# Optimization experiments

Hardware: AMD Instinct MI355X
Metric: run time of the kernel (lower is better)

The kernel has to match this reference:

```python
import jax, jax.numpy as jnp
import numpy as np

NG = 1024      # graphs
NPG = 128      # nodes per graph (forced by lin1 = Linear(128*hid, 128))
N = NG * NPG   # 131072 nodes
DEG = 16       # avg in-graph degree
E = N * DEG    # 2,097,152 edges
IN, H = 4, 64


def setup_inputs() -> dict:
    key = jax.random.key(0)
    ks = jax.random.split(key, 24)
    x = jax.random.normal(ks[0], (N, IN), jnp.float32)
    # edges constrained within each 128-node graph
    src = jax.random.randint(ks[1], (E,), 0, NPG)
    dst = jax.random.randint(ks[2], (E,), 0, NPG)
    off = jnp.repeat(jnp.arange(NG, dtype=jnp.int32) * NPG, NPG * DEG)
    edge_index = jnp.stack([src.astype(jnp.int32) + off, dst.astype(jnp.int32) + off])
    g = lambda k, shp, fan: jax.random.normal(k, shp, jnp.float32) / np.float32(np.sqrt(fan))
    return {
        "x": x, "edge_index": edge_index,
        # GATv2Conv(4->64)
        "Wl": g(ks[3], (IN, H), IN), "bl": jnp.zeros((H,), jnp.float32),
        "Wr": g(ks[4], (IN, H), IN), "br": jnp.zeros((H,), jnp.float32),
        "att_v2": g(ks[5], (H,), H), "b_v2": jnp.zeros((H,), jnp.float32),
        # GATConv #1 (64->64)
        "Wg1": g(ks[6], (H, H), H), "as1": g(ks[7], (H,), H),
        "ad1": g(ks[8], (H,), H), "bg1": jnp.zeros((H,), jnp.float32),
        # GATConv #2 (64->64)
        "Wg2": g(ks[9], (H, H), H), "as2": g(ks[10], (H,), H),
        "ad2": g(ks[11], (H,), H), "bg2": jnp.zeros((H,), jnp.float32),
        # LayerNorm(64)
        "ln_g": jnp.ones((H,), jnp.float32), "ln_b": jnp.zeros((H,), jnp.float32),
        # heads: Linear(128*64 -> 128), Linear(128 -> 1)
        "W1": g(ks[12], (NPG * H, 128), NPG * H), "b1": jnp.zeros((128,), jnp.float32),
        "W2": g(ks[13], (128, 1), 128), "b2": jnp.zeros((1,), jnp.float32),
    }


def _seg_softmax(logits, seg):
    # stable softmax over edges grouped by destination node
    m = jax.ops.segment_max(logits, seg, num_segments=N)
    ex = jnp.exp(logits - m[seg])
    s = jax.ops.segment_sum(ex, seg, num_segments=N)
    return ex / (s[seg] + 1e-16)


def _gatv2(x, src, dst, Wl, bl, Wr, br, att, bias):
    xl = x @ Wl + bl                       # source transform [N,H]
    xr = x @ Wr + br                       # target transform [N,H]
    e = jax.nn.leaky_relu(xl[src] + xr[dst], 0.2) @ att   # [E]
    a = _seg_softmax(e, dst)
    out = jax.ops.segment_sum(a[:, None] * xl[src], dst, num_segments=N)
    return out + bias


def _gat(x, src, dst, W, a_src, a_dst, bias):
    # GATConv default: add self-loops
    loop = jnp.arange(N, dtype=src.dtype)
    s2 = jnp.concatenate([src, loop]); d2 = jnp.concatenate([dst, loop])
    xw = x @ W                             # [N,H]
    al_s = xw @ a_src; al_d = xw @ a_dst   # per-node attention halves [N]
    e = jax.nn.leaky_relu(al_s[s2] + al_d[d2], 0.2)
    a = _seg_softmax(e, d2)
    out = jax.ops.segment_sum(a[:, None] * xw[s2], d2, num_segments=N)
    return out + bias


def _layernorm(x, g, b, eps=1e-5):
    mu = jnp.mean(x, -1, keepdims=True)
    var = jnp.mean(jnp.square(x - mu), -1, keepdims=True)
    return (x - mu) * jax.lax.rsqrt(var + eps) * g + b


def reference(x, edge_index, Wl, bl, Wr, br, att_v2, b_v2,
              Wg1, as1, ad1, bg1, Wg2, as2, ad2, bg2,
              ln_g, ln_b, W1, b1, W2, b2):
    src, dst = edge_index[0], edge_index[1]
    h = jax.nn.leaky_relu(_gatv2(x, src, dst, Wl, bl, Wr, br, att_v2, b_v2), 0.01)
    h = _layernorm(h, ln_g, ln_b)
    h = jax.nn.relu(_gat(h, src, dst, Wg1, as1, ad1, bg1))
    h = jax.nn.relu(_gat(h, src, dst, Wg2, as2, ad2, bg2))
    # linearize: batch is sorted with exactly NPG nodes per graph -> reshape
    h = h.reshape(NG, NPG * H)
    h = jax.nn.leaky_relu(h @ W1 + b1, 0.01)
    return jax.nn.sigmoid(h @ W2 + b2)     # [NG, 1]
```

## Files before the change

### kernel.cpp

```cpp
#include <hip/hip_runtime.h>
#include <hip/hip_bf16.h>

#define NGRAPH 1024
#define NPG 128
#define NTOT (NGRAPH*NPG)
#define EPG 2048
#define ETOT (NTOT*16)
#define HD 64

typedef unsigned int uint;
typedef unsigned short ushort_t;
typedef __attribute__((ext_vector_type(8))) short s8v;
typedef __attribute__((ext_vector_type(4))) float f32x4;

#define MFMA16 __builtin_amdgcn_mfma_f32_16x16x32_bf16

__device__ __forceinline__ float lrelu(float x, float s){ return fmaxf(x, x*s); }
__device__ __forceinline__ float b2lo(uint u){ return __uint_as_float(u << 16); }
__device__ __forceinline__ float b2hi(uint u){ return __uint_as_float(u & 0xFFFF0000u); }
__device__ __forceinline__ uint pkbf(float a, float b){
  union { __hip_bfloat162 h; uint u; } t;
  t.h = __hip_bfloat162{__float2bfloat16(a), __float2bfloat16(b)};
  return t.u;
}
__device__ __forceinline__ ushort_t bfb(float v){
  __hip_bfloat16 h = __float2bfloat16(v);
  union { __hip_bfloat16 h; ushort_t u; } t; t.h = h; return t.u;
}
union U4S8 { uint4 u; s8v s; };
__device__ __forceinline__ s8v bcs8(uint4 u){ U4S8 t; t.u = u; return t.s; }

#define DPP_ADD(v, ctrl) ((v) + __int_as_float(__builtin_amdgcn_update_dpp(0, __float_as_int(v), (ctrl), 0xF, 0xF, false)))

__device__ __forceinline__ int oswz(int r, int p){ return (r<<5) | ((((p>>2) ^ (r & 7))<<2) | (p & 3)); }
__device__ __forceinline__ int obase(int r, int oc){ return (r<<5) | (((oc) ^ (r & 7))<<2); }
__device__ __forceinline__ int sstg(int r, int c){ return (r<<5) | ((c ^ r) & 31); }

#define O_F   0
#define O_W   4096
#define O_EV  6144
#define O_ED  7168
#define O_X   8192
#define O_SOF 8704
#define O_SPO 8833
#define O_NMV 8961
#define O_SSE 9089
#define O_ALS 9217
#define O_ALD 9345
#define O_WAS 9476
#define O_WAD 9540
#define SM_SZ 9604

#define GF16(s, a) { \
    uint4 q0 = *(uint4*)&SM[O_F + obase((s), 2*qf+0)]; \
    uint4 q1 = *(uint4*)&SM[O_F + obase((s), 2*qf+1)]; \
    c0.x += (a)*b2lo(q0.x); c0.y += (a)*b2hi(q0.x); c0.z += (a)*b2lo(q0.y); c0.w += (a)*b2hi(q0.y); \
    c1.x += (a)*b2lo(q0.z); c1.y += (a)*b2hi(q0.z); c1.z += (a)*b2lo(q0.w); c1.w += (a)*b2hi(q0.w); \
    c2.x += (a)*b2lo(q1.x); c2.y += (a)*b2hi(q1.x); c2.z += (a)*b2lo(q1.y); c2.w += (a)*b2hi(q1.y); \
    c3.x += (a)*b2lo(q1.z); c3.y += (a)*b2hi(q1.z); c3.z += (a)*b2lo(q1.w); c3.w += (a)*b2hi(q1.w); }

#define STF16(d) { \
    sXl[oswz((d), qf*8+0)] = pkbf(c0.x,c0.y); sXl[oswz((d), qf*8+1)] = pkbf(c0.z,c0.w); \
    sXl[oswz((d), qf*8+2)] = pkbf(c1.x,c1.y); sXl[oswz((d), qf*8+3)] = pkbf(c1.z,c1.w); \
    sXl[oswz((d), qf*8+4)] = pkbf(c2.x,c2.y); sXl[oswz((d), qf*8+5)] = pkbf(c2.z,c2.w); \
    sXl[oswz((d), qf*8+6)] = pkbf(c3.x,c3.y); sXl[oswz((d), qf*8+7)] = pkbf(c3.z,c3.w); }
#define STG16(d) { \
    stg[sstg((d), qf*8+0)] = pkbf(c0.x,c0.y); stg[sstg((d), qf*8+1)] = pkbf(c0.z,c0.w); \
    stg[sstg((d), qf*8+2)] = pkbf(c1.x,c1.y); stg[sstg((d), qf*8+3)] = pkbf(c1.z,c1.w); \
    stg[sstg((d), qf*8+4)] = pkbf(c2.x,c2.y); stg[sstg((d), qf*8+5)] = pkbf(c2.z,c2.w); \
    stg[sstg((d), qf*8+6)] = pkbf(c3.x,c3.y); stg[sstg((d), qf*8+7)] = pkbf(c3.z,c3.w); }

__global__ void __launch_bounds__(256, 4) gnn_fused(
    const float* __restrict__ x, const int* __restrict__ ei,
    const float* __restrict__ Wl, const float* __restrict__ bl,
    const float* __restrict__ Wr, const float* __restrict__ br,
    const float* __restrict__ att, const float* __restrict__ bv2,
    const float* __restrict__ Wg1, const float* __restrict__ as1,
    const float* __restrict__ ad1, const float* __restrict__ bg1,
    const float* __restrict__ Wg2, const float* __restrict__ as2,
    const float* __restrict__ ad2, const float* __restrict__ bg2,
    const float* __restrict__ lng, const float* __restrict__ lnb,
    uint* __restrict__ hout)
{
  __shared__ uint SM[SM_SZ];
  uint*      sXl  = SM + O_F;
  _Float16*  evh  = (_Float16*)(SM + O_EV);
  ushort_t*  edsd = (ushort_t*)(SM + O_ED);
  int*       soff = (int*)(SM + O_SOF);
  int*       spos = (int*)(SM + O_SPO);
  float*     nmv  = (float*)(SM + O_NMV);
  float*     sse  = (float*)(SM + O_SSE);
  float*     als  = (float*)(SM + O_ALS);
  float*     ald  = (float*)(SM + O_ALD);
  float*     was  = (float*)(SM + O_WAS);
  float*     wad  = (float*)(SM + O_WAD);
  ushort_t*  sH16 = (ushort_t*)(SM + O_F);
  ushort_t*  wg16 = (ushort_t*)(SM + O_W);
  float*     lgf  = (float*)(SM + O_W);
  uint*      stg  = SM + O_W;

  const int g    = blockIdx.x;
  const int tid  = threadIdx.x;
  const int lane = tid & 63;
  const int wv   = tid >> 6;
  const int lw   = lane & 15;
  const int lq   = lane >> 4;
  const int oc   = lane & 7;
  const int ebase = g * EPG;

  if (tid < NPG) spos[tid] = 0;
  __syncthreads();
  for (int e = tid; e < EPG; e += 256)
    atomicAdd(&spos[ei[ETOT + ebase + e] - g*NPG], 1);
  __syncthreads();
  if (wv == 0) {
    int c0 = spos[lane], c1 = spos[lane + 64];
    #pragma unroll
    for (int o = 1; o < 64; o <<= 1) { int t = __shfl_up(c0, o); if (lane >= o) c0 += t; }
    #pragma unroll
    for (int o = 1; o < 64; o <<= 1) { int t = __shfl_up(c1, o); if (lane >= o) c1 += t; }
    int tot0 = __shfl(c0, 63);
    soff[lane + 1]  = c0;
    soff[lane + 65] = c1 + tot0;
    if (lane == 0) soff[0] = 0;
  }
  __syncthreads();
  if (tid < NPG) spos[tid] = soff[tid];
  __syncthreads();
  for (int e = tid; e < EPG; e += 256) {
    int s = ei[ebase + e] - g*NPG;
    int d = ei[ETOT + ebase + e] - g*NPG;
    int p = atomicAdd(&spos[d], 1);
    edsd[p] = (ushort_t)(s | (d << 8));
  }

  {
    const float4* x4g = (const float4*)x + (size_t)g * NPG;
    float4* sx4w = (float4*)(SM + O_X);
    if (tid < NPG) sx4w[tid] = x4g[tid];
    const int pl = lane & 31, hb = lane >> 5;
    const float2 wl0 = *(const float2*)&Wl[0*64 + 2*pl];
    const float2 wl1 = *(const float2*)&Wl[1*64 + 2*pl];
    const float2 wl2 = *(const float2*)&Wl[2*64 + 2*pl];
    const float2 wl3 = *(const float2*)&Wl[3*64 + 2*pl];
    const float2 blp = *(const float2*)&bl[2*pl];
    for (int st = 0; st < 16; st++) {
      int i = st*8 + wv*2 + hb;
      float4 xi = x4g[i];
      float l0 = blp.x + xi.x*wl0.x + xi.y*wl1.x + xi.z*wl2.x + xi.w*wl3.x;
      float l1 = blp.y + xi.x*wl0.y + xi.y*wl1.y + xi.z*wl2.y + xi.w*wl3.y;
      sXl[oswz(i, pl)] = pkbf(l0, l1);
    }
  }
  __syncthreads();

  {
    const float4* sx4 = (const float4*)(SM + O_X);
    const int g16 = tid >> 4;
    float4 w0 = *(const float4*)&Wr[0*64 + lw*4];
    float4 w1 = *(const float4*)&Wr[1*64 + lw*4];
    float4 w2 = *(const float4*)&Wr[2*64 + lw*4];
    float4 w3 = *(const float4*)&Wr[3*64 + lw*4];
    float4 brv = *(const float4*)&br[lw*4];
    float4 atv = *(const float4*)&att[lw*4];
    for (int it = 0; it < 8; it++) {
      int d = it*16 + g16;
      float4 xd = sx4[d];
      float4 xr;
      xr.x = brv.x + xd.x*w0.x + xd.y*w1.x + xd.z*w2.x + xd.w*w3.x;
      xr.y = brv.y + xd.x*w0.y + xd.y*w1.y + xd.z*w2.y + xd.w*w3.y;
      xr.z = brv.z + xd.x*w0.z + xd.y*w1.z + xd.z*w2.z + xd.w*w3.z;
      xr.w = brv.w + xd.x*w0.w + xd.y*w1.w + xd.z*w2.w + xd.w*w3.w;
      int p0 = soff[d], p1 = soff[d+1];
      for (int p = p0; p < p1; p++) {
        int s = edsd[p] & 127;
        uint2 ql = *(uint2*)&SM[O_F + oswz(s, 2*lw)];
        float e, v;
        v = b2lo(ql.x)+xr.x; e  = lrelu(v,0.2f)*atv.x;
        v = b2hi(ql.x)+xr.y; e += lrelu(v,0.2f)*atv.y;
        v = b2lo(ql.y)+xr.z; e += lrelu(v,0.2f)*atv.z;
        v = b2hi(ql.y)+xr.w; e += lrelu(v,0.2f)*atv.w;
        e = DPP_ADD(e, 0x111); e = DPP_ADD(e, 0x112);
        e = DPP_ADD(e, 0x114); e = DPP_ADD(e, 0x118);
        if (lw == 15) lgf[p] = e;
      }
    }
  }
  __syncthreads();

  {
    const int g16 = tid >> 4, sl = tid & 15;
    for (int it = 0; it < 8; it++) {
      int d = it*16 + g16;
      int p0 = soff[d], p1 = soff[d+1];
      float m = -1e30f;
      for (int p = p0 + sl; p < p1; p += 16) m = fmaxf(m, lgf[p]);
      #pragma unroll
      for (int o = 1; o < 16; o <<= 1) m = fmaxf(m, __shfl_xor(m, o));
      float ssum = 0.f;
      for (int p = p0 + sl; p < p1; p += 16) {
        float ex = __expf(lgf[p] - m); ssum += ex; evh[p] = (_Float16)ex;
      }
      #pragma unroll
      for (int o = 1; o < 16; o <<= 1) ssum += __shfl_xor(ssum, o);
      if (sl == 0) nmv[d] = 1.f / (ssum + 1e-16f);
    }
  }
  __syncthreads();

  {
    const int rr = tid >> 2, qf = tid & 3;
    auto doRow = [&](int d, int toStage) {
      int p0 = soff[d], p1 = soff[d+1];
      float nmv_d = nmv[d];
      f32x4 c0={0,0,0,0}, c1={0,0,0,0}, c2={0,0,0,0}, c3={0,0,0,0};
      for (int p = p0; p < p1; p++) {
        int s = edsd[p] & 127;
        float a = nmv_d * (float)evh[p];
        GF16(s, a)
      }
      float s1 = 0.f, s2 = 0.f;
      #define BRELN(cv, j) { \
        float4 bq = *(const float4*)&bv2[qf*16 + 4*(j)]; \
        cv.x = lrelu(cv.x + bq.x, 0.01f); cv.y = lrelu(cv.y + bq.y, 0.01f); \
        cv.z = lrelu(cv.z + bq.z, 0.01f); cv.w = lrelu(cv.w + bq.w, 0.01f); \
        s1 += cv.x + cv.y + cv.z + cv.w; \
        s2 += cv.x*cv.x + cv.y*cv.y + cv.z*cv.z + cv.w*cv.w; }
      BRELN(c0,0) BRELN(c1,1) BRELN(c2,2) BRELN(c3,3)
      #undef BRELN
      s1 += __shfl_xor(s1, 1); s2 += __shfl_xor(s2, 1);
      s1 += __shfl_xor(s1, 2); s2 += __shfl_xor(s2, 2);
      float mu  = s1 * 0.015625f;
      float var = s2 * 0.015625f - mu*mu;
      float rs  = rsqrtf(var + 1e-5f);
      #define LNAP(cv, j) { \
        float4 gq = *(const float4*)&lng[qf*16 + 4*(j)]; \
        float4 bq = *(const float4*)&lnb[qf*16 + 4*(j)]; \
        cv.x = (cv.x-mu)*rs*gq.x + bq.x; cv.y = (cv.y-mu)*rs*gq.y + bq.y; \
        cv.z = (cv.z-mu)*rs*gq.z + bq.z; cv.w = (cv.w-mu)*rs*gq.w + bq.w; }
      LNAP(c0,0) LNAP(c1,1) LNAP(c2,2) LNAP(c3,3)
      #undef LNAP
      if (toStage) {
        STG16(d)
      } else {
        __syncthreads();
        STF16(d)
      }
    };
    doRow(rr, 1);
    doRow(64 + rr, 0);
    #pragma unroll
    for (int i = 0; i < 8; i++) {
      int idx = tid + i*256; int r = idx >> 5, c = idx & 31;
      sXl[oswz(r, c)] = stg[sstg(r, c)];
    }
  }
  __syncthreads();

  for (int layer = 0; layer < 2; layer++) {
    const float* Wg  = layer ? Wg2 : Wg1;
    const float* avs = layer ? as2 : as1;
    const float* avd = layer ? ad2 : ad1;
    const float* bg  = layer ? bg2 : bg1;

    if (tid < 128) {
      const float* av = (tid < 64) ? avs : avd;
      float* dst = (tid < 64) ? was : wad;
      int k = tid & 63;
      float acc = 0.f;
      #pragma unroll
      for (int jj = 0; jj < 16; jj++) {
        float4 w = *(const float4*)&Wg[k*64 + jj*4];
        float4 a = *(const float4*)&av[jj*4];
        acc += w.x*a.x + w.y*a.y + w.z*a.z + w.w*a.w;
      }
      dst[k] = acc;
    } else {
      int t2 = tid - 128;
      #pragma unroll
      for (int i = 0; i < 8; i++) {
        int idx = t2 + i*128;
        int k = idx >> 4, j4 = (idx & 15)*4;
        float4 w = *(const float4*)&Wg[k*64 + j4];
        wg16[oswz(j4+0, k>>1)*2 + (k&1)] = bfb(w.x);
        wg16[oswz(j4+1, k>>1)*2 + (k&1)] = bfb(w.y);
        wg16[oswz(j4+2, k>>1)*2 + (k&1)] = bfb(w.z);
        wg16[oswz(j4+3, k>>1)*2 + (k&1)] = bfb(w.w);
      }
    }
    __syncthreads();

    {
      float4 ws0 = *(float4*)&was[oc*8], ws1 = *(float4*)&was[oc*8 + 4];
      float4 wd0 = *(float4*)&wad[oc*8], wd1 = *(float4*)&wad[oc*8 + 4];
      for (int ps = 0; ps < 4; ps++) {
        int n = ps*32 + (tid >> 3);
        uint4 qv = *(uint4*)&SM[O_F + obase(n, oc)];
        float f0=b2lo(qv.x), f1=b2hi(qv.x), f2=b2lo(qv.y), f3=b2hi(qv.y);
        float f4=b2lo(qv.z), f5=b2hi(qv.z), f6=b2lo(qv.w), f7=b2hi(qv.w);
        float sa = f0*ws0.x+f1*ws0.y+f2*ws0.z+f3*ws0.w+f4*ws1.x+f5*ws1.y+f6*ws1.z+f7*ws1.w;
        float sd = f0*wd0.x+f1*wd0.y+f2*wd0.z+f3*wd0.w+f4*wd1.x+f5*wd1.y+f6*wd1.z+f7*wd1.w;
        sa = DPP_ADD(sa, 0x111); sa = DPP_ADD(sa, 0x112); sa = DPP_ADD(sa, 0x114);
        sd = DPP_ADD(sd, 0x111); sd = DPP_ADD(sd, 0x112); sd = DPP_ADD(sd, 0x114);
        if ((lane & 7) == 7) { als[n] = sa; ald[n] = sd; }
      }
    }
    __syncthreads();

    {
      const int r0 = 32*wv;
      uint4 a00 = *(uint4*)&SM[O_F + obase(r0+lw,    lq  )];
      uint4 a01 = *(uint4*)&SM[O_F + obase(r0+lw,    4+lq)];
      uint4 a10 = *(uint4*)&SM[O_F + obase(r0+16+lw, lq  )];
      uint4 a11 = *(uint4*)&SM[O_F + obase(r0+16+lw, 4+lq)];
      #pragma unroll
      for (int nt = 0; nt < 4; nt++) {
        uint4 b0 = *(uint4*)&SM[O_W + obase(nt*16+lw, lq  )];
        uint4 b1 = *(uint4*)&SM[O_W + obase(nt*16+lw, 4+lq)];
        f32x4 z = {0.f,0.f,0.f,0.f};
        f32x4 c0 = MFMA16(bcs8(a00), bcs8(b0), z, 0, 0, 0);
        c0 = MFMA16(bcs8(a01), bcs8(b1), c0, 0, 0, 0);
        f32x4 c1 = MFMA16(bcs8(a10), bcs8(b0), z, 0, 0, 0);
        c1 = MFMA16(bcs8(a11), bcs8(b1), c1, 0, 0, 0);
        int col = nt*16 + lw;
        #pragma unroll
        for (int rg = 0; rg < 4; rg++) {
          sH16[oswz(r0 + lq*4 + rg,      col>>1)*2 + (col&1)] = bfb(c0[rg]);
          sH16[oswz(r0 + 16 + lq*4 + rg, col>>1)*2 + (col&1)] = bfb(c1[rg]);
        }
      }
    }
    {
      const int g16 = tid >> 4, sl = tid & 15;
      for (int it = 0; it < 8; it++) {
        int d = it*16 + g16;
        int p0 = soff[d], p1 = soff[d+1];
        float adv = ald[d];
        float se = lrelu(als[d] + adv, 0.2f);
        float m = se;
        for (int p = p0 + sl; p < p1; p += 16)
          m = fmaxf(m, lrelu(als[edsd[p] & 127] + adv, 0.2f));
        #pragma unroll
        for (int o = 1; o < 16; o <<= 1) m = fmaxf(m, __shfl_xor(m, o));
        float ex0 = __expf(se - m);
        float ssum = 0.f;
        for (int p = p0 + sl; p < p1; p += 16) {
          float ex = __expf(lrelu(als[edsd[p] & 127] + adv, 0.2f) - m);
          ssum += ex; evh[p] = (_Float16)ex;
        }
        #pragma unroll
        for (int o = 1; o < 16; o <<= 1) ssum += __shfl_xor(ssum, o);
        if (sl == 0) { nmv[d] = 1.f / (ssum + ex0 + 1e-16f); sse[d] = ex0; }
      }
    }
    __syncthreads();

    {
      const int rr = tid >> 2, qf = tid & 3;
      auto doRow = [&](int d, int toStage) {
        int p0 = soff[d], p1 = soff[d+1];
        float nmv_d = nmv[d];
        f32x4 c0={0,0,0,0}, c1={0,0,0,0}, c2={0,0,0,0}, c3={0,0,0,0};
        {
          float a0 = sse[d] * nmv_d;
          GF16(d, a0)
        }
        for (int p = p0; p < p1; p++) {
          int s = edsd[p] & 127;
          float a = nmv_d * (float)evh[p];
          GF16(s, a)
        }
        #define BREL2(cv, j) { \
          float4 bq = *(const float4*)&bg[qf*16 + 4*(j)]; \
          cv.x = fmaxf(cv.x + bq.x, 0.f); cv.y = fmaxf(cv.y + bq.y, 0.f); \
          cv.z = fmaxf(cv.z + bq.z, 0.f); cv.w = fmaxf(cv.w + bq.w, 0.f); }
        BREL2(c0,0) BREL2(c1,1) BREL2(c2,2) BREL2(c3,3)
        #undef BREL2
        if (toStage) {
          STG16(d)
        } else {
          __syncthreads();
          STF16(d)
        }
      };
      doRow(rr, 1);
      doRow(64 + rr, 0);
      #pragma unroll
      for (int i = 0; i < 8; i++) {
        int idx = tid + i*256; int r = idx >> 5, c = idx & 31;
        sXl[oswz(r, c)] = stg[sstg(r, c)];
      }
    }
    __syncthreads();
  }

  {
    uint* hg = hout + (size_t)g * 4096;
    #pragma unroll
    for (int i = 0; i < 16; i++) {
      int idx = tid + i*256;
      hg[idx] = SM[O_F + oswz(idx >> 5, idx & 31)];
    }
  }
}

__global__ __launch_bounds__(256) void w1_transpose(const float* __restrict__ W1,
                                                    uint* __restrict__ w1t)
{
  __shared__ float sw[64*130];
  const int tid = threadIdx.x;
  const int k0 = blockIdx.x * 64;
  #pragma unroll
  for (int i = 0; i < 8; i++) {
    int idx = tid + i*256;
    int r = idx >> 5, c4 = (idx & 31)*4;
    *(float4*)&sw[r*130 + c4] = *(const float4*)&W1[(size_t)(k0+r)*128 + c4];
  }
  __syncthreads();
  #pragma unroll
  for (int i = 0; i < 16; i++) {
    int idx = tid + i*256;
    int c = idx >> 5, kp = idx & 31;
    w1t[(size_t)c*4096 + (k0>>1) + kp] = pkbf(sw[(2*kp)*130 + c], sw[(2*kp+1)*130 + c]);
  }
}

__global__ __launch_bounds__(256) void head_gemm(
    const uint* __restrict__ hbuf, const uint* __restrict__ w1t,
    float* __restrict__ partial)
{
  __shared__ uint sAh[2048];
  __shared__ uint sBh[4096];
  const int tid = threadIdx.x, lane = tid & 63, wv = tid >> 6;
  const int lw = lane & 15, lq = lane >> 4;
  const int g0 = blockIdx.x * 64;
  const int ks = blockIdx.y;
  f32x4 acc[8];
  #pragma unroll
  for (int i = 0; i < 8; i++) acc[i] = f32x4{0.f,0.f,0.f,0.f};

  for (int ch = 0; ch < 8; ch++) {
    int pb = ks*256 + ch*32;
    #pragma unroll
    for (int i = 0; i < 2; i++) {
      int idx = tid + i*256; int r = idx >> 3, q4 = idx & 7;
      uint4 v = *(const uint4*)&hbuf[(size_t)(g0+r)*4096 + pb + q4*4];
      *(uint4*)&sAh[(r<<5) | ((q4 ^ (r & 7))<<2)] = v;
    }
    #pragma unroll
    for (int i = 0; i < 4; i++) {
      int idx = tid + i*256; int r = idx >> 3, q4 = idx & 7;
      uint4 v = *(const uint4*)&w1t[(size_t)r*4096 + pb + q4*4];
      *(uint4*)&sBh[(r<<5) | ((q4 ^ (r & 7))<<2)] = v;
    }
    __syncthreads();
    int ra = 16*wv + lw;
    s8v a0 = bcs8(*(uint4*)&sAh[obase(ra, lq)]);
    s8v a1 = bcs8(*(uint4*)&sAh[obase(ra, 4+lq)]);
    #pragma unroll
    for (int nt = 0; nt < 8; nt++) {
      int c = nt*16 + lw;
      s8v b0 = bcs8(*(uint4*)&sBh[obase(c, lq)]);
      s8v b1 = bcs8(*(uint4*)&sBh[obase(c, 4+lq)]);
      acc[nt] = MFMA16(a0, b0, acc[nt], 0, 0, 0);
      acc[nt] = MFMA16(a1, b1, acc[nt], 0, 0, 0);
    }
    __syncthreads();
  }
  float* pp = partial + (size_t)ks*131072;
  #pragma unroll
  for (int nt = 0; nt < 8; nt++) {
    int c = nt*16 + lw;
    int r0 = g0 + 16*wv + lq*4;
    #pragma unroll
    for (int rg = 0; rg < 4; rg++)
      pp[(size_t)(r0+rg)*128 + c] = acc[nt][rg];
  }
}

__global__ __launch_bounds__(64) void head_out(
    const float* __restrict__ partial, const float* __restrict__ b1,
    const float* __restrict__ W2, const float* __restrict__ b2,
    float* __restrict__ out)
{
  const int g = blockIdx.x;
  const int l = threadIdx.x;
  float v0 = b1[l], v1 = b1[64 + l];
  #pragma unroll
  for (int s = 0; s < 16; s++) {
    v0 += partial[(size_t)s*131072 + g*128 + l];
    v1 += partial[(size_t)s*131072 + g*128 + 64 + l];
  }
  float sum = lrelu(v0, 0.01f)*W2[l] + lrelu(v1, 0.01f)*W2[64 + l];
  #pragma unroll
  for (int m = 32; m > 0; m >>= 1) sum += __shfl_xor(sum, m);
  if (l == 0) out[g] = 1.f / (1.f + __expf(-(sum + b2[0])));
}

extern "C" void kernel_launch(void* const* d_in, const int* in_sizes, int n_in,
                              void* d_out, int out_size, void* d_ws, size_t ws_size,
                              hipStream_t stream) {
  const float* x   = (const float*)d_in[0];
  const int*   ei  = (const int*)  d_in[1];
  const float* Wl  = (const float*)d_in[2];
  const float* bl_ = (const float*)d_in[3];
  const float* Wr  = (const float*)d_in[4];
  const float* br_ = (const float*)d_in[5];
  const float* att = (const float*)d_in[6];
  const float* bv2 = (const float*)d_in[7];
  const float* Wg1 = (const float*)d_in[8];
  const float* as1 = (const float*)d_in[9];
  const float* ad1 = (const float*)d_in[10];
  const float* bg1 = (const float*)d_in[11];
  const float* Wg2 = (const float*)d_in[12];
  const float* as2 = (const float*)d_in[13];
  const float* ad2 = (const float*)d_in[14];
  const float* bg2 = (const float*)d_in[15];
  const float* lng = (const float*)d_in[16];
  const float* lnb = (const float*)d_in[17];
  const float* W1  = (const float*)d_in[18];
  const float* b1  = (const float*)d_in[19];
  const float* W2  = (const float*)d_in[20];
  const float* b2  = (const float*)d_in[21];
  float* out = (float*)d_out;

  uint*  hbuf    = (uint*)d_ws;
  float* partial = (float*)((char*)d_ws + (size_t)16*1024*1024);
  uint*  w1t     = (uint*)((char*)d_ws + (size_t)24*1024*1024);

  w1_transpose<<<128, 256, 0, stream>>>(W1, w1t);
  gnn_fused<<<NGRAPH, 256, 0, stream>>>(x, ei, Wl, bl_, Wr, br_, att, bv2,
      Wg1, as1, ad1, bg1, Wg2, as2, ad2, bg2, lng, lnb, hbuf);
  head_gemm<<<dim3(16, 16), 256, 0, stream>>>(hbuf, w1t, partial);
  head_out<<<NGRAPH, 64, 0, stream>>>(partial, b1, W2, b2, out);
}
```

Measured before the change: 285.9 us.

## Assign one row per thread pair and stage partial accumulators in fp16 LDS

Changes the aggregation mapping from four threads per row over two row passes to two threads per row in a single pass. Each thread covers 32 features by walking the edge list twice, once per 16-feature half. Between the walks it parks the first half's accumulators in fp16 in LDS to keep register pressure down. This drops the staged transpose copy and the mid-row barrier, and each thread now reads the edge list once per destination row instead of once per row pass. In exchange, edge metadata is read twice per thread and the staged values lose precision through fp16 rounding.

```diff
diff --git a/kernel.cpp b/kernel.cpp
--- a/kernel.cpp
+++ b/kernel.cpp
@@ -27,6 +27,16 @@
   __hip_bfloat16 h = __float2bfloat16(v);
   union { __hip_bfloat16 h; ushort_t u; } t; t.h = h; return t.u;
 }
+__device__ __forceinline__ uint pkh2(float a, float b){
+  union { _Float16 h[2]; uint u; } t;
+  t.h[0] = (_Float16)a; t.h[1] = (_Float16)b; return t.u;
+}
+__device__ __forceinline__ float h2lo(uint u){
+  union { _Float16 h[2]; uint u_; } t; t.u_ = u; return (float)t.h[0];
+}
+__device__ __forceinline__ float h2hi(uint u){
+  union { _Float16 h[2]; uint u_; } t; t.u_ = u; return (float)t.h[1];
+}
 union U4S8 { uint4 u; s8v s; };
 __device__ __forceinline__ s8v bcs8(uint4 u){ U4S8 t; t.u = u; return t.s; }
 
@@ -34,7 +44,6 @@
 
 __device__ __forceinline__ int oswz(int r, int p){ return (r<<5) | ((((p>>2) ^ (r & 7))<<2) | (p & 3)); }
 __device__ __forceinline__ int obase(int r, int oc){ return (r<<5) | (((oc) ^ (r & 7))<<2); }
-__device__ __forceinline__ int sstg(int r, int c){ return (r<<5) | ((c ^ r) & 31); }
 
 #define O_F   0
 #define O_W   4096
@@ -51,24 +60,35 @@
 #define O_WAD 9540
 #define SM_SZ 9604
 
-#define GF16(s, a) { \
-    uint4 q0 = *(uint4*)&SM[O_F + obase((s), 2*qf+0)]; \
-    uint4 q1 = *(uint4*)&SM[O_F + obase((s), 2*qf+1)]; \
+#define GQ16(s, a, qa, qb) { \
+    uint4 q0 = *(uint4*)&SM[O_F + obase((s), (qa))]; \
+    uint4 q1 = *(uint4*)&SM[O_F + obase((s), (qb))]; \
     c0.x += (a)*b2lo(q0.x); c0.y += (a)*b2hi(q0.x); c0.z += (a)*b2lo(q0.y); c0.w += (a)*b2hi(q0.y); \
     c1.x += (a)*b2lo(q0.z); c1.y += (a)*b2hi(q0.z); c1.z += (a)*b2lo(q0.w); c1.w += (a)*b2hi(q0.w); \
     c2.x += (a)*b2lo(q1.x); c2.y += (a)*b2hi(q1.x); c2.z += (a)*b2lo(q1.y); c2.w += (a)*b2hi(q1.y); \
     c3.x += (a)*b2lo(q1.z); c3.y += (a)*b2hi(q1.z); c3.z += (a)*b2lo(q1.w); c3.w += (a)*b2hi(q1.w); }
 
-#define STF16(d) { \
-    sXl[oswz((d), qf*8+0)] = pkbf(c0.x,c0.y); sXl[oswz((d), qf*8+1)] = pkbf(c0.z,c0.w); \
-    sXl[oswz((d), qf*8+2)] = pkbf(c1.x,c1.y); sXl[oswz((d), qf*8+3)] = pkbf(c1.z,c1.w); \
-    sXl[oswz((d), qf*8+4)] = pkbf(c2.x,c2.y); sXl[oswz((d), qf*8+5)] = pkbf(c2.z,c2.w); \
-    sXl[oswz((d), qf*8+6)] = pkbf(c3.x,c3.y); sXl[oswz((d), qf*8+7)] = pkbf(c3.z,c3.w); }
-#define STG16(d) { \
-    stg[sstg((d), qf*8+0)] = pkbf(c0.x,c0.y); stg[sstg((d), qf*8+1)] = pkbf(c0.z,c0.w); \
-    stg[sstg((d), qf*8+2)] = pkbf(c1.x,c1.y); stg[sstg((d), qf*8+3)] = pkbf(c1.z,c1.w); \
-    stg[sstg((d), qf*8+4)] = pkbf(c2.x,c2.y); stg[sstg((d), qf*8+5)] = pkbf(c2.z,c2.w); \
-    stg[sstg((d), qf*8+6)] = pkbf(c3.x,c3.y); stg[sstg((d), qf*8+7)] = pkbf(c3.z,c3.w); }
+#define STG_A() { \
+    stgu[0*256+tid] = pkh2(c0.x,c0.y); stgu[1*256+tid] = pkh2(c0.z,c0.w); \
+    stgu[2*256+tid] = pkh2(c1.x,c1.y); stgu[3*256+tid] = pkh2(c1.z,c1.w); \
+    stgu[4*256+tid] = pkh2(c2.x,c2.y); stgu[5*256+tid] = pkh2(c2.z,c2.w); \
+    stgu[6*256+tid] = pkh2(c3.x,c3.y); stgu[7*256+tid] = pkh2(c3.z,c3.w); }
+#define LDG_A() \
+    f32x4 a0, a1, a2, a3; \
+    { uint u0=stgu[0*256+tid], u1=stgu[1*256+tid]; a0 = f32x4{h2lo(u0),h2hi(u0),h2lo(u1),h2hi(u1)}; } \
+    { uint u0=stgu[2*256+tid], u1=stgu[3*256+tid]; a1 = f32x4{h2lo(u0),h2hi(u0),h2lo(u1),h2hi(u1)}; } \
+    { uint u0=stgu[4*256+tid], u1=stgu[5*256+tid]; a2 = f32x4{h2lo(u0),h2hi(u0),h2lo(u1),h2hi(u1)}; } \
+    { uint u0=stgu[6*256+tid], u1=stgu[7*256+tid]; a3 = f32x4{h2lo(u0),h2hi(u0),h2lo(u1),h2hi(u1)}; }
+
+#define STF_AB(d) { \
+    sXl[oswz((d), hf*16+ 0)] = pkbf(a0.x,a0.y); sXl[oswz((d), hf*16+ 1)] = pkbf(a0.z,a0.w); \
+    sXl[oswz((d), hf*16+ 2)] = pkbf(a1.x,a1.y); sXl[oswz((d), hf*16+ 3)] = pkbf(a1.z,a1.w); \
+    sXl[oswz((d), hf*16+ 4)] = pkbf(a2.x,a2.y); sXl[oswz((d), hf*16+ 5)] = pkbf(a2.z,a2.w); \
+    sXl[oswz((d), hf*16+ 6)] = pkbf(a3.x,a3.y); sXl[oswz((d), hf*16+ 7)] = pkbf(a3.z,a3.w); \
+    sXl[oswz((d), hf*16+ 8)] = pkbf(c0.x,c0.y); sXl[oswz((d), hf*16+ 9)] = pkbf(c0.z,c0.w); \
+    sXl[oswz((d), hf*16+10)] = pkbf(c1.x,c1.y); sXl[oswz((d), hf*16+11)] = pkbf(c1.z,c1.w); \
+    sXl[oswz((d), hf*16+12)] = pkbf(c2.x,c2.y); sXl[oswz((d), hf*16+13)] = pkbf(c2.z,c2.w); \
+    sXl[oswz((d), hf*16+14)] = pkbf(c3.x,c3.y); sXl[oswz((d), hf*16+15)] = pkbf(c3.z,c3.w); }
 
 __global__ void __launch_bounds__(256, 4) gnn_fused(
     const float* __restrict__ x, const int* __restrict__ ei,
@@ -97,7 +117,7 @@
   ushort_t*  sH16 = (ushort_t*)(SM + O_F);
   ushort_t*  wg16 = (ushort_t*)(SM + O_W);
   float*     lgf  = (float*)(SM + O_W);
-  uint*      stg  = SM + O_W;
+  uint*      stgu = SM + O_W;
 
   const int g    = blockIdx.x;
   const int tid  = threadIdx.x;
@@ -209,51 +229,49 @@
   __syncthreads();
 
   {
-    const int rr = tid >> 2, qf = tid & 3;
-    auto doRow = [&](int d, int toStage) {
-      int p0 = soff[d], p1 = soff[d+1];
-      float nmv_d = nmv[d];
+    const int d = tid >> 1, hf = tid & 1;
+    const int p0 = soff[d], p1 = soff[d+1];
+    const float nmv_d = nmv[d];
+    {
       f32x4 c0={0,0,0,0}, c1={0,0,0,0}, c2={0,0,0,0}, c3={0,0,0,0};
       for (int p = p0; p < p1; p++) {
         int s = edsd[p] & 127;
         float a = nmv_d * (float)evh[p];
-        GF16(s, a)
-      }
-      float s1 = 0.f, s2 = 0.f;
-      #define BRELN(cv, j) { \
-        float4 bq = *(const float4*)&bv2[qf*16 + 4*(j)]; \
-        cv.x = lrelu(cv.x + bq.x, 0.01f); cv.y = lrelu(cv.y + bq.y, 0.01f); \
-        cv.z = lrelu(cv.z + bq.z, 0.01f); cv.w = lrelu(cv.w + bq.w, 0.01f); \
-        s1 += cv.x + cv.y + cv.z + cv.w; \
-        s2 += cv.x*cv.x + cv.y*cv.y + cv.z*cv.z + cv.w*cv.w; }
-      BRELN(c0,0) BRELN(c1,1) BRELN(c2,2) BRELN(c3,3)
-      #undef BRELN
-      s1 += __shfl_xor(s1, 1); s2 += __shfl_xor(s2, 1);
-      s1 += __shfl_xor(s1, 2); s2 += __shfl_xor(s2, 2);
-      float mu  = s1 * 0.015625f;
-      float var = s2 * 0.015625f - mu*mu;
-      float rs  = rsqrtf(var + 1e-5f);
-      #define LNAP(cv, j) { \
-        float4 gq = *(const float4*)&lng[qf*16 + 4*(j)]; \
-        float4 bq = *(const float4*)&lnb[qf*16 + 4*(j)]; \
-        cv.x = (cv.x-mu)*rs*gq.x + bq.x; cv.y = (cv.y-mu)*rs*gq.y + bq.y; \
-        cv.z = (cv.z-mu)*rs*gq.z + bq.z; cv.w = (cv.w-mu)*rs*gq.w + bq.w; }
-      LNAP(c0,0) LNAP(c1,1) LNAP(c2,2) LNAP(c3,3)
-      #undef LNAP
-      if (toStage) {
-        STG16(d)
-      } else {
-        __syncthreads();
-        STF16(d)
-      }
-    };
-    doRow(rr, 1);
-    doRow(64 + rr, 0);
-    #pragma unroll
-    for (int i = 0; i < 8; i++) {
-      int idx = tid + i*256; int r = idx >> 5, c = idx & 31;
-      sXl[oswz(r, c)] = stg[sstg(r, c)];
-    }
+        GQ16(s, a, 4*hf+0, 4*hf+1)
+      }
+      STG_A()
+    }
+    f32x4 c0={0,0,0,0}, c1={0,0,0,0}, c2={0,0,0,0}, c3={0,0,0,0};
+    for (int p = p0; p < p1; p++) {
+      int s = edsd[p] & 127;
+      float a = nmv_d * (float)evh[p];
+      GQ16(s, a, 4*hf+2, 4*hf+3)
+    }
+    LDG_A()
+    float s1 = 0.f, s2 = 0.f;
+    #define BLN(cv, base, j) { \
+      float4 bq = *(const float4*)&bv2[hf*32 + (base) + 4*(j)]; \
+      cv.x = lrelu(cv.x + bq.x, 0.01f); cv.y = lrelu(cv.y + bq.y, 0.01f); \
+      cv.z = lrelu(cv.z + bq.z, 0.01f); cv.w = lrelu(cv.w + bq.w, 0.01f); \
+      s1 += cv.x + cv.y + cv.z + cv.w; \
+      s2 += cv.x*cv.x + cv.y*cv.y + cv.z*cv.z + cv.w*cv.w; }
+    BLN(a0,0,0) BLN(a1,0,1) BLN(a2,0,2) BLN(a3,0,3)
+    BLN(c0,16,0) BLN(c1,16,1) BLN(c2,16,2) BLN(c3,16,3)
+    #undef BLN
+    s1 += __shfl_xor(s1, 1); s2 += __shfl_xor(s2, 1);
+    float mu  = s1 * 0.015625f;
+    float var = s2 * 0.015625f - mu*mu;
+    float rs  = rsqrtf(var + 1e-5f);
+    #define LNA(cv, base, j) { \
+      float4 gq = *(const float4*)&lng[hf*32 + (base) + 4*(j)]; \
+      float4 bq = *(const float4*)&lnb[hf*32 + (base) + 4*(j)]; \
+      cv.x = (cv.x-mu)*rs*gq.x + bq.x; cv.y = (cv.y-mu)*rs*gq.y + bq.y; \
+      cv.z = (cv.z-mu)*rs*gq.z + bq.z; cv.w = (cv.w-mu)*rs*gq.w + bq.w; }
+    LNA(a0,0,0) LNA(a1,0,1) LNA(a2,0,2) LNA(a3,0,3)
+    LNA(c0,16,0) LNA(c1,16,1) LNA(c2,16,2) LNA(c3,16,3)
+    #undef LNA
+    __syncthreads();
+    STF_AB(d)
   }
   __syncthreads();
 
@@ -356,40 +374,37 @@
     __syncthreads();
 
     {
-      const int rr = tid >> 2, qf = tid & 3;
-      auto doRow = [&](int d, int toStage) {
-        int p0 = soff[d], p1 = soff[d+1];
-        float nmv_d = nmv[d];
+      const int d = tid >> 1, hf = tid & 1;
+      const int p0 = soff[d], p1 = soff[d+1];
+      const float nmv_d = nmv[d];
+      const float slw = sse[d] * nmv_d;
+      {
         f32x4 c0={0,0,0,0}, c1={0,0,0,0}, c2={0,0,0,0}, c3={0,0,0,0};
-        {
-          float a0 = sse[d] * nmv_d;
-          GF16(d, a0)
-        }
+        GQ16(d, slw, 4*hf+0, 4*hf+1)
         for (int p = p0; p < p1; p++) {
           int s = edsd[p] & 127;
           float a = nmv_d * (float)evh[p];
-          GF16(s, a)
+          GQ16(s, a, 4*hf+0, 4*hf+1)
         }
-        #define BREL2(cv, j) { \
-          float4 bq = *(const float4*)&bg[qf*16 + 4*(j)]; \
-          cv.x = fmaxf(cv.x + bq.x, 0.f); cv.y = fmaxf(cv.y + bq.y, 0.f); \
-          cv.z = fmaxf(cv.z + bq.z, 0.f); cv.w = fmaxf(cv.w + bq.w, 0.f); }
-        BREL2(c0,0) BREL2(c1,1) BREL2(c2,2) BREL2(c3,3)
-        #undef BREL2
-        if (toStage) {
-          STG16(d)
-        } else {
-          __syncthreads();
-          STF16(d)
-        }
-      };
-      doRow(rr, 1);
-      doRow(64 + rr, 0);
-      #pragma unroll
-      for (int i = 0; i < 8; i++) {
-        int idx = tid + i*256; int r = idx >> 5, c = idx & 31;
-        sXl[oswz(r, c)] = stg[sstg(r, c)];
-      }
+        STG_A()
+      }
+      f32x4 c0={0,0,0,0}, c1={0,0,0,0}, c2={0,0,0,0}, c3={0,0,0,0};
+      GQ16(d, slw, 4*hf+2, 4*hf+3)
+      for (int p = p0; p < p1; p++) {
+        int s = edsd[p] & 127;
+        float a = nmv_d * (float)evh[p];
+        GQ16(s, a, 4*hf+2, 4*hf+3)
+      }
+      LDG_A()
+      #define BRL(cv, base, j) { \
+        float4 bq = *(const float4*)&bg[hf*32 + (base) + 4*(j)]; \
+        cv.x = fmaxf(cv.x + bq.x, 0.f); cv.y = fmaxf(cv.y + bq.y, 0.f); \
+        cv.z = fmaxf(cv.z + bq.z, 0.f); cv.w = fmaxf(cv.w + bq.w, 0.f); }
+      BRL(a0,0,0) BRL(a1,0,1) BRL(a2,0,2) BRL(a3,0,3)
+      BRL(c0,16,0) BRL(c1,16,1) BRL(c2,16,2) BRL(c3,16,3)
+      #undef BRL
+      __syncthreads();
+      STF_AB(d)
     }
     __syncthreads();
   }
```

After: 289.6 us. No clear change (+1.3%).
